# Kernel tuning notes

Measured on AMD Instinct MI355X. Metric: run time of the kernel, lower is better.

The kernel has to match this reference:

```python
import jax, jax.numpy as jnp
import numpy as np

NBINS = 256
NCH = 3


def _channel_hists(img):
    """img: [B, 3, H, W] float with values in [0, 256).
    Returns [3, 256] histogram counts, summed over the batch (matches
    cv2.calcHist per channel accumulated over images)."""
    idx = jnp.clip(img, 0.0, 255.0).astype(jnp.int32)          # bin = floor(v)
    offs = (jnp.arange(NCH, dtype=jnp.int32) * NBINS)[None, :, None, None]
    flat = (idx + offs).reshape(-1)                             # [B*3*H*W]
    h = jnp.zeros(NCH * NBINS, dtype=img.dtype).at[flat].add(1.0)
    return h.reshape(NCH, NBINS)


def _bhattacharyya_sum(h1, h2):
    """OpenCV HISTCMP_BHATTACHARYYA per channel, summed over channels.
    d = sqrt(1 - sum(sqrt(H1*H2)) / (N * sqrt(mean(H1)*mean(H2))))"""
    s = jnp.sum(jnp.sqrt(h1 * h2), axis=-1)                     # [3]
    denom = jnp.sqrt(h1.mean(-1) * h2.mean(-1)) * NBINS         # [3]
    d = jnp.sqrt(jnp.maximum(1.0 - s / denom, 0.0))
    return jnp.sum(d)


def setup_inputs() -> dict:
    key = jax.random.key(0)
    k1, k2 = jax.random.split(key)
    shape = (32, 3, 512, 512)
    # pixel values in [0, 256) like real image data
    inp = jax.random.uniform(k1, shape, dtype=jnp.float32) * 256.0
    lab = jax.random.uniform(k2, shape, dtype=jnp.float32) * 256.0
    return {"input": inp, "label": lab}


def reference(input, label):
    h_in = _channel_hists(input)    # [3, 256]
    h_lb = _channel_hists(label)    # [3, 256]
    return _bhattacharyya_sum(h_in, h_lb)
```

## Files before the change

kernel.cpp:

```cpp
#include <hip/hip_runtime.h>

#define NBINS 256
#define NCH 3
#define NHIST (2 * NCH * NBINS)
#define HW4 65536
#define BATCH 32
#define BLOCKS_PER_JOB 256
#define THREADS 256

__device__ __forceinline__ void batch4(unsigned int* lbase, float4 v) {
    const int b0 = (int)fminf(fmaxf(v.x, 0.f), 255.f);
    const int b1 = (int)fminf(fmaxf(v.y, 0.f), 255.f);
    const int b2 = (int)fminf(fmaxf(v.z, 0.f), 255.f);
    const int b3 = (int)fminf(fmaxf(v.w, 0.f), 255.f);
    const int w0 = b0 >> 2, w1 = b1 >> 2, w2 = b2 >> 2, w3 = b3 >> 2;
    unsigned int i0 = 1u << ((b0 & 3) << 3);
    unsigned int i1 = 1u << ((b1 & 3) << 3);
    unsigned int i2 = 1u << ((b2 & 3) << 3);
    unsigned int i3 = 1u << ((b3 & 3) << 3);
    unsigned int* const p0 = lbase + w0 * 64;
    unsigned int* const p1 = lbase + w1 * 64;
    unsigned int* const p2 = lbase + w2 * 64;
    unsigned int* const p3 = lbase + w3 * 64;
    const unsigned int r0 = *p0;
    const unsigned int r1 = *p1;
    const unsigned int r2 = *p2;
    const unsigned int r3 = *p3;
    if (w0 == w1) { i1 += i0; i0 = 0; }
    if (w0 == w2) { i2 += i0; i0 = 0; }
    if (w0 == w3) { i3 += i0; i0 = 0; }
    if (w1 == w2) { i2 += i1; i1 = 0; }
    if (w1 == w3) { i3 += i1; i1 = 0; }
    if (w2 == w3) { i3 += i2; i2 = 0; }
    *p0 = r0 + i0;
    *p1 = r1 + i1;
    *p2 = r2 + i2;
    *p3 = r3 + i3;
}

__global__ __launch_bounds__(THREADS) void hist_kernel(
    const float* __restrict__ a, const float* __restrict__ b,
    unsigned int* __restrict__ gh) {
    __shared__ unsigned int sh[16384];
    const int tid  = threadIdx.x;
    const int wave = tid >> 6;
    const int lane = tid & 63;

    uint4* shv = (uint4*)sh;
    #pragma unroll
    for (int i = 0; i < 16; ++i)
        shv[tid + i * THREADS] = make_uint4(0u, 0u, 0u, 0u);
    __syncthreads();

    const int job        = blockIdx.x >> 8;
    const int blockInJob = blockIdx.x & 255;
    const int arr = job / NCH;
    const int ch  = job % NCH;

    const float4* __restrict__ src = (const float4*)(arr ? b : a);
    unsigned int* const lbase = &sh[wave * 4096 + lane];
    const unsigned pos = ((unsigned)blockInJob << 8) | (unsigned)tid;

    for (int it = 0; it < BATCH / 4; ++it) {
        const int bt = it << 2;
        const float4 v0 = src[(unsigned)(((bt + 0) * NCH + ch) << 16) | pos];
        const float4 v1 = src[(unsigned)(((bt + 1) * NCH + ch) << 16) | pos];
        const float4 v2 = src[(unsigned)(((bt + 2) * NCH + ch) << 16) | pos];
        const float4 v3 = src[(unsigned)(((bt + 3) * NCH + ch) << 16) | pos];
        batch4(lbase, v0);
        batch4(lbase, v1);
        batch4(lbase, v2);
        batch4(lbase, v3);
    }
    __syncthreads();

    unsigned int sum = 0;
    const int grp = tid >> 2;
    const int sh8 = (tid & 3) << 3;
    #pragma unroll
    for (int w = 0; w < 4; ++w) {
        const unsigned int* base = &sh[w * 4096 + grp * 64];
        #pragma unroll
        for (int c = 0; c < 16; ++c) {
            const int cc = (c + tid) & 15;
            const uint4 q = *(const uint4*)(base + cc * 4);
            sum += ((q.x >> sh8) & 0xFFu) + ((q.y >> sh8) & 0xFFu)
                 + ((q.z >> sh8) & 0xFFu) + ((q.w >> sh8) & 0xFFu);
        }
    }
    atomicAdd(&gh[(arr * NCH + ch) * NBINS + tid], sum);
}

__device__ __forceinline__ double block_reduce256(double v, double* sh4) {
    const int t = threadIdx.x;
    const int lane = t & 63, w = t >> 6;
    #pragma unroll
    for (int o = 32; o > 0; o >>= 1) v += __shfl_down(v, o, 64);
    if (lane == 0) sh4[w] = v;
    __syncthreads();
    double r = sh4[0] + sh4[1] + sh4[2] + sh4[3];
    __syncthreads();
    return r;
}

__global__ __launch_bounds__(256) void bhat_kernel(
    const unsigned int* __restrict__ gh, float* __restrict__ out) {
    __shared__ double sh4[4];
    const int t = threadIdx.x;
    double result = 0.0;
    #pragma unroll
    for (int ch = 0; ch < NCH; ++ch) {
        const double h1 = (double)gh[ch * NBINS + t];
        const double h2 = (double)gh[(NCH + ch) * NBINS + t];
        const double s  = block_reduce256(sqrt(h1 * h2), sh4);
        const double s1 = block_reduce256(h1, sh4);
        const double s2 = block_reduce256(h2, sh4);
        const double denom = sqrt((s1 / (double)NBINS) * (s2 / (double)NBINS)) * (double)NBINS;
        const double v = 1.0 - s / denom;
        result += sqrt(v > 0.0 ? v : 0.0);
    }
    if (t == 0) out[0] = (float)result;
}

extern "C" void kernel_launch(void* const* d_in, const int* in_sizes, int n_in,
                              void* d_out, int out_size, void* d_ws, size_t ws_size,
                              hipStream_t stream) {
    const float* input = (const float*)d_in[0];
    const float* label = (const float*)d_in[1];
    float* out = (float*)d_out;
    unsigned int* gh = (unsigned int*)d_ws;

    hipMemsetAsync(gh, 0, NHIST * sizeof(unsigned int), stream);

    hist_kernel<<<6 * BLOCKS_PER_JOB, THREADS, 0, stream>>>(input, label, gh);
    bhat_kernel<<<1, 256, 0, stream>>>(gh, out);
}
```

Before: 218.5 us.

## Share LDS byte-counter histograms between lane pairs with DPP merge and prefetch

```diff
diff --git a/kernel.cpp b/kernel.cpp
--- a/kernel.cpp
+++ b/kernel.cpp
@@ -4,11 +4,15 @@
 #define NCH 3
 #define NHIST (2 * NCH * NBINS)
 #define HW4 65536
-#define BATCH 32
-#define BLOCKS_PER_JOB 256
+#define BLOCKS_PER_JOB 512
 #define THREADS 256
+#define STEP (2 * NCH * HW4)
 
-__device__ __forceinline__ void batch4(unsigned int* lbase, float4 v) {
+__device__ __forceinline__ int dppswap(int v) {
+    return __builtin_amdgcn_mov_dpp(v, 0xB1, 0xF, 0xF, false);
+}
+
+__device__ __forceinline__ void process4(unsigned int* __restrict__ base, float4 v) {
     const int b0 = (int)fminf(fmaxf(v.x, 0.f), 255.f);
     const int b1 = (int)fminf(fmaxf(v.y, 0.f), 255.f);
     const int b2 = (int)fminf(fmaxf(v.z, 0.f), 255.f);
@@ -18,10 +22,10 @@
     unsigned int i1 = 1u << ((b1 & 3) << 3);
     unsigned int i2 = 1u << ((b2 & 3) << 3);
     unsigned int i3 = 1u << ((b3 & 3) << 3);
-    unsigned int* const p0 = lbase + w0 * 64;
-    unsigned int* const p1 = lbase + w1 * 64;
-    unsigned int* const p2 = lbase + w2 * 64;
-    unsigned int* const p3 = lbase + w3 * 64;
+    unsigned int* const p0 = base + w0 * 32;
+    unsigned int* const p1 = base + w1 * 32;
+    unsigned int* const p2 = base + w2 * 32;
+    unsigned int* const p3 = base + w3 * 32;
     const unsigned int r0 = *p0;
     const unsigned int r1 = *p1;
     const unsigned int r2 = *p2;
@@ -32,63 +36,103 @@
     if (w1 == w2) { i2 += i1; i1 = 0; }
     if (w1 == w3) { i3 += i1; i1 = 0; }
     if (w2 == w3) { i3 += i2; i2 = 0; }
+    const int pw0 = dppswap(w0), pw1 = dppswap(w1);
+    const int pw2 = dppswap(w2), pw3 = dppswap(w3);
+    const unsigned pi0 = (unsigned)dppswap((int)i0);
+    const unsigned pi1 = (unsigned)dppswap((int)i1);
+    const unsigned pi2 = (unsigned)dppswap((int)i2);
+    const unsigned pi3 = (unsigned)dppswap((int)i3);
+    i0 += (w0 == pw0 ? pi0 : 0u) + (w0 == pw1 ? pi1 : 0u)
+        + (w0 == pw2 ? pi2 : 0u) + (w0 == pw3 ? pi3 : 0u);
+    i1 += (w1 == pw0 ? pi0 : 0u) + (w1 == pw1 ? pi1 : 0u)
+        + (w1 == pw2 ? pi2 : 0u) + (w1 == pw3 ? pi3 : 0u);
+    i2 += (w2 == pw0 ? pi0 : 0u) + (w2 == pw1 ? pi1 : 0u)
+        + (w2 == pw2 ? pi2 : 0u) + (w2 == pw3 ? pi3 : 0u);
+    i3 += (w3 == pw0 ? pi0 : 0u) + (w3 == pw1 ? pi1 : 0u)
+        + (w3 == pw2 ? pi2 : 0u) + (w3 == pw3 ? pi3 : 0u);
     *p0 = r0 + i0;
     *p1 = r1 + i1;
     *p2 = r2 + i2;
     *p3 = r3 + i3;
 }
 
-__global__ __launch_bounds__(THREADS) void hist_kernel(
+__global__ __launch_bounds__(THREADS, 5) void hist_kernel(
     const float* __restrict__ a, const float* __restrict__ b,
     unsigned int* __restrict__ gh) {
-    __shared__ unsigned int sh[16384];
+    __shared__ unsigned int sh[8192];
     const int tid  = threadIdx.x;
     const int wave = tid >> 6;
     const int lane = tid & 63;
 
     uint4* shv = (uint4*)sh;
     #pragma unroll
-    for (int i = 0; i < 16; ++i)
+    for (int i = 0; i < 8; ++i)
         shv[tid + i * THREADS] = make_uint4(0u, 0u, 0u, 0u);
     __syncthreads();
 
-    const int job        = blockIdx.x >> 8;
-    const int blockInJob = blockIdx.x & 255;
+    const int job = blockIdx.x / BLOCKS_PER_JOB;
+    const int bij = blockIdx.x % BLOCKS_PER_JOB;
     const int arr = job / NCH;
     const int ch  = job % NCH;
 
-    const float4* __restrict__ src = (const float4*)(arr ? b : a);
-    unsigned int* const lbase = &sh[wave * 4096 + lane];
-    const unsigned pos = ((unsigned)blockInJob << 8) | (unsigned)tid;
+    const float4* __restrict__ src4 = (const float4*)(arr ? b : a);
+    unsigned int* const base = &sh[wave * 2048 + (lane >> 1)];
 
-    for (int it = 0; it < BATCH / 4; ++it) {
-        const int bt = it << 2;
-        const float4 v0 = src[(unsigned)(((bt + 0) * NCH + ch) << 16) | pos];
-        const float4 v1 = src[(unsigned)(((bt + 1) * NCH + ch) << 16) | pos];
-        const float4 v2 = src[(unsigned)(((bt + 2) * NCH + ch) << 16) | pos];
-        const float4 v3 = src[(unsigned)(((bt + 3) * NCH + ch) << 16) | pos];
-        batch4(lbase, v0);
-        batch4(lbase, v1);
-        batch4(lbase, v2);
-        batch4(lbase, v3);
+    const unsigned tg  = ((unsigned)bij << 8) | (unsigned)tid;
+    const unsigned hi  = tg >> 16;
+    const unsigned pos = tg & (HW4 - 1);
+    const unsigned base_idx = hi * (NCH * HW4) + (unsigned)ch * HW4 + pos;
+
+    float4 c0 = src4[base_idx + 0u * STEP];
+    float4 c1 = src4[base_idx + 1u * STEP];
+    float4 c2 = src4[base_idx + 2u * STEP];
+    float4 c3 = src4[base_idx + 3u * STEP];
+    #pragma unroll
+    for (int g2 = 0; g2 < 4; ++g2) {
+        float4 n0, n1, n2, n3;
+        if (g2 < 3) {
+            const unsigned k = (unsigned)(4 * g2 + 4);
+            n0 = src4[base_idx + (k + 0u) * STEP];
+            n1 = src4[base_idx + (k + 1u) * STEP];
+            n2 = src4[base_idx + (k + 2u) * STEP];
+            n3 = src4[base_idx + (k + 3u) * STEP];
+        }
+        process4(base, c0);
+        process4(base, c1);
+        process4(base, c2);
+        process4(base, c3);
+        if (g2 < 3) { c0 = n0; c1 = n1; c2 = n2; c3 = n3; }
     }
     __syncthreads();
 
-    unsigned int sum = 0;
-    const int grp = tid >> 2;
-    const int sh8 = (tid & 3) << 3;
-    #pragma unroll
-    for (int w = 0; w < 4; ++w) {
-        const unsigned int* base = &sh[w * 4096 + grp * 64];
+    {
+        const unsigned int* rbase = &sh[wave * 2048 + lane * 32];
+        unsigned lo = 0u, hiS = 0u;
         #pragma unroll
-        for (int c = 0; c < 16; ++c) {
-            const int cc = (c + tid) & 15;
-            const uint4 q = *(const uint4*)(base + cc * 4);
-            sum += ((q.x >> sh8) & 0xFFu) + ((q.y >> sh8) & 0xFFu)
-                 + ((q.z >> sh8) & 0xFFu) + ((q.w >> sh8) & 0xFFu);
+        for (int c = 0; c < 8; ++c) {
+            const int cc = (c + lane) & 7;
+            const uint4 q = *(const uint4*)(rbase + cc * 4);
+            lo  += (q.x & 0x00FF00FFu) + (q.y & 0x00FF00FFu)
+                 + (q.z & 0x00FF00FFu) + (q.w & 0x00FF00FFu);
+            hiS += ((q.x >> 8) & 0x00FF00FFu) + ((q.y >> 8) & 0x00FF00FFu)
+                 + ((q.z >> 8) & 0x00FF00FFu) + ((q.w >> 8) & 0x00FF00FFu);
         }
+        sh[wave * 2048 + lane]      = lo;
+        sh[wave * 2048 + 64 + lane] = hiS;
     }
-    atomicAdd(&gh[(arr * NCH + ch) * NBINS + tid], sum);
+    __syncthreads();
+
+    {
+        const int g = tid >> 2, byte = tid & 3;
+        const int off = (byte & 1) ? 64 : 0;
+        unsigned s = 0u;
+        #pragma unroll
+        for (int q = 0; q < 4; ++q) {
+            const unsigned v = sh[q * 2048 + off + g];
+            s += (byte & 2) ? (v >> 16) : (v & 0xFFFFu);
+        }
+        atomicAdd(&gh[(arr * NCH + ch) * NBINS + tid], s);
+    }
 }
 
 __device__ __forceinline__ double block_reduce256(double v, double* sh4) {
```

Measured after the change: 226.7 us. 1.04x slower.

## Split histogram into per-array kernels with LDS atomics and prefetched loads

Applied to the files above, without the earlier changes.

```diff
diff --git a/kernel.cpp b/kernel.cpp
--- a/kernel.cpp
+++ b/kernel.cpp
@@ -4,9 +4,87 @@
 #define NCH 3
 #define NHIST (2 * NCH * NBINS)
 #define HW4 65536
-#define BATCH 32
-#define BLOCKS_PER_JOB 256
 #define THREADS 256
+#define BLOCKS_PER_JOB 512
+#define STEP (2 * NCH * HW4)
+
+
+__global__ __launch_bounds__(THREADS) void hist_atomic(
+    const float* __restrict__ src, unsigned int* __restrict__ gh) {
+    __shared__ unsigned int sh[8192];
+    const int tid  = threadIdx.x;
+    const int wave = tid >> 6;
+    const int lane = tid & 63;
+    const int pair = lane >> 1;
+
+    uint4* shv = (uint4*)sh;
+    #pragma unroll
+    for (int i = 0; i < 8; ++i)
+        shv[tid + i * THREADS] = make_uint4(0u, 0u, 0u, 0u);
+    __syncthreads();
+
+    const int ch  = blockIdx.x / BLOCKS_PER_JOB;
+    const int bij = blockIdx.x % BLOCKS_PER_JOB;
+
+    const float4* __restrict__ src4 = (const float4*)src;
+    unsigned int* const base = &sh[wave * 2048 + pair * 64];
+
+    const unsigned tg  = ((unsigned)bij << 8) | (unsigned)tid;
+    const unsigned hi  = tg >> 16;
+    const unsigned pos = tg & (HW4 - 1);
+    const unsigned base_idx = hi * (NCH * HW4) + (unsigned)ch * HW4 + pos;
+
+    #define ATOM1(x) do { \
+        const int _b = (int)fminf(fmaxf((x), 0.f), 255.f); \
+        atomicAdd(&base[_b >> 2], 1u << ((_b & 3) << 3)); } while (0)
+    #define ATOM4(v) do { ATOM1((v).x); ATOM1((v).y); ATOM1((v).z); ATOM1((v).w); } while (0)
+
+    float4 c0 = src4[base_idx + 0u * STEP];
+    float4 c1 = src4[base_idx + 1u * STEP];
+    float4 c2 = src4[base_idx + 2u * STEP];
+    float4 c3 = src4[base_idx + 3u * STEP];
+    #pragma unroll
+    for (int g2 = 0; g2 < 4; ++g2) {
+        float4 n0, n1, n2, n3;
+        if (g2 < 3) {
+            const unsigned k = (unsigned)(4 * g2 + 4);
+            n0 = src4[base_idx + (k + 0u) * STEP];
+            n1 = src4[base_idx + (k + 1u) * STEP];
+            n2 = src4[base_idx + (k + 2u) * STEP];
+            n3 = src4[base_idx + (k + 3u) * STEP];
+        }
+        ATOM4(c0); ATOM4(c1); ATOM4(c2); ATOM4(c3);
+        if (g2 < 3) { c0 = n0; c1 = n1; c2 = n2; c3 = n3; }
+    }
+    __syncthreads();
+
+    {
+        const unsigned int* rb = &sh[wave * 2048];
+        unsigned lo = 0u, hiS = 0u;
+        #pragma unroll
+        for (int p = 0; p < 32; ++p) {
+            const int pp = (p + lane) & 31;
+            const unsigned v = rb[pp * 64 + lane];
+            lo  += v & 0x00FF00FFu;
+            hiS += (v >> 8) & 0x00FF00FFu;
+        }
+        sh[wave * 2048 + lane]      = lo;
+        sh[wave * 2048 + 64 + lane] = hiS;
+    }
+    __syncthreads();
+
+    {
+        const int grp = tid >> 2, byte = tid & 3;
+        const int off = (byte & 1) ? 64 : 0;
+        unsigned s = 0u;
+        #pragma unroll
+        for (int q = 0; q < 4; ++q) {
+            const unsigned v = sh[q * 2048 + off + grp];
+            s += (byte & 2) ? (v >> 16) : (v & 0xFFFFu);
+        }
+        atomicAdd(&gh[ch * NBINS + tid], s);
+    }
+}
 
 __device__ __forceinline__ void batch4(unsigned int* lbase, float4 v) {
     const int b0 = (int)fminf(fmaxf(v.x, 0.f), 255.f);
@@ -38,9 +116,8 @@
     *p3 = r3 + i3;
 }
 
-__global__ __launch_bounds__(THREADS) void hist_kernel(
-    const float* __restrict__ a, const float* __restrict__ b,
-    unsigned int* __restrict__ gh) {
+__global__ __launch_bounds__(THREADS) void hist_rmw(
+    const float* __restrict__ src, unsigned int* __restrict__ gh) {
     __shared__ unsigned int sh[16384];
     const int tid  = threadIdx.x;
     const int wave = tid >> 6;
@@ -52,25 +129,36 @@
         shv[tid + i * THREADS] = make_uint4(0u, 0u, 0u, 0u);
     __syncthreads();
 
-    const int job        = blockIdx.x >> 8;
-    const int blockInJob = blockIdx.x & 255;
-    const int arr = job / NCH;
-    const int ch  = job % NCH;
-
-    const float4* __restrict__ src = (const float4*)(arr ? b : a);
+    const int ch  = blockIdx.x / BLOCKS_PER_JOB;
+    const int bij = blockIdx.x % BLOCKS_PER_JOB;
+
+    const float4* __restrict__ src4 = (const float4*)src;
     unsigned int* const lbase = &sh[wave * 4096 + lane];
-    const unsigned pos = ((unsigned)blockInJob << 8) | (unsigned)tid;
-
-    for (int it = 0; it < BATCH / 4; ++it) {
-        const int bt = it << 2;
-        const float4 v0 = src[(unsigned)(((bt + 0) * NCH + ch) << 16) | pos];
-        const float4 v1 = src[(unsigned)(((bt + 1) * NCH + ch) << 16) | pos];
-        const float4 v2 = src[(unsigned)(((bt + 2) * NCH + ch) << 16) | pos];
-        const float4 v3 = src[(unsigned)(((bt + 3) * NCH + ch) << 16) | pos];
-        batch4(lbase, v0);
-        batch4(lbase, v1);
-        batch4(lbase, v2);
-        batch4(lbase, v3);
+
+    const unsigned tg  = ((unsigned)bij << 8) | (unsigned)tid;
+    const unsigned hi  = tg >> 16;
+    const unsigned pos = tg & (HW4 - 1);
+    const unsigned base_idx = hi * (NCH * HW4) + (unsigned)ch * HW4 + pos;
+
+    float4 c0 = src4[base_idx + 0u * STEP];
+    float4 c1 = src4[base_idx + 1u * STEP];
+    float4 c2 = src4[base_idx + 2u * STEP];
+    float4 c3 = src4[base_idx + 3u * STEP];
+    #pragma unroll
+    for (int g2 = 0; g2 < 4; ++g2) {
+        float4 n0, n1, n2, n3;
+        if (g2 < 3) {
+            const unsigned k = (unsigned)(4 * g2 + 4);
+            n0 = src4[base_idx + (k + 0u) * STEP];
+            n1 = src4[base_idx + (k + 1u) * STEP];
+            n2 = src4[base_idx + (k + 2u) * STEP];
+            n3 = src4[base_idx + (k + 3u) * STEP];
+        }
+        batch4(lbase, c0);
+        batch4(lbase, c1);
+        batch4(lbase, c2);
+        batch4(lbase, c3);
+        if (g2 < 3) { c0 = n0; c1 = n1; c2 = n2; c3 = n3; }
     }
     __syncthreads();
 
@@ -88,7 +176,7 @@
                  + ((q.z >> sh8) & 0xFFu) + ((q.w >> sh8) & 0xFFu);
         }
     }
-    atomicAdd(&gh[(arr * NCH + ch) * NBINS + tid], sum);
+    atomicAdd(&gh[(NCH + ch) * NBINS + tid], sum);
 }
 
 __device__ __forceinline__ double block_reduce256(double v, double* sh4) {
@@ -132,6 +220,7 @@
 
     hipMemsetAsync(gh, 0, NHIST * sizeof(unsigned int), stream);
 
-    hist_kernel<<<6 * BLOCKS_PER_JOB, THREADS, 0, stream>>>(input, label, gh);
+    hist_atomic<<<NCH * BLOCKS_PER_JOB, THREADS, 0, stream>>>(input, gh);
+    hist_rmw   <<<NCH * BLOCKS_PER_JOB, THREADS, 0, stream>>>(label, gh);
     bhat_kernel<<<1, 256, 0, stream>>>(gh, out);
 }
```

Result: slower. 229.5 us (+5.0%).

## Split histogram work between LDS packed counters and per-wave global atomic copies

Applied to the files above, without the earlier changes.

```diff
diff --git a/kernel.cpp b/kernel.cpp
--- a/kernel.cpp
+++ b/kernel.cpp
@@ -4,9 +4,14 @@
 #define NCH 3
 #define NHIST (2 * NCH * NBINS)
 #define HW4 65536
-#define BATCH 32
-#define BLOCKS_PER_JOB 256
 #define THREADS 256
+#define BLOCKS_PER_JOB 512
+#define NJOBS 6
+#define STEP (2 * NCH * HW4)
+#define WAVES_PER_JOB (BLOCKS_PER_JOB * 4)
+#define NCOPIES (NJOBS * WAVES_PER_JOB)
+#define PRIV_OFF 2048
+
 
 __device__ __forceinline__ void batch4(unsigned int* lbase, float4 v) {
     const int b0 = (int)fminf(fmaxf(v.x, 0.f), 255.f);
@@ -38,9 +43,16 @@
     *p3 = r3 + i3;
 }
 
+__device__ __forceinline__ void gatom4(unsigned int* __restrict__ g, float4 v) {
+    atomicAdd(&g[(int)fminf(fmaxf(v.x, 0.f), 255.f)], 1u);
+    atomicAdd(&g[(int)fminf(fmaxf(v.y, 0.f), 255.f)], 1u);
+    atomicAdd(&g[(int)fminf(fmaxf(v.z, 0.f), 255.f)], 1u);
+    atomicAdd(&g[(int)fminf(fmaxf(v.w, 0.f), 255.f)], 1u);
+}
+
 __global__ __launch_bounds__(THREADS) void hist_kernel(
     const float* __restrict__ a, const float* __restrict__ b,
-    unsigned int* __restrict__ gh) {
+    unsigned int* __restrict__ priv, unsigned int* __restrict__ gh) {
     __shared__ unsigned int sh[16384];
     const int tid  = threadIdx.x;
     const int wave = tid >> 6;
@@ -52,25 +64,40 @@
         shv[tid + i * THREADS] = make_uint4(0u, 0u, 0u, 0u);
     __syncthreads();
 
-    const int job        = blockIdx.x >> 8;
-    const int blockInJob = blockIdx.x & 255;
+    const int job = blockIdx.x >> 9;
+    const int bij = blockIdx.x & 511;
     const int arr = job / NCH;
     const int ch  = job % NCH;
 
-    const float4* __restrict__ src = (const float4*)(arr ? b : a);
+    const float4* __restrict__ src4 = (const float4*)(arr ? b : a);
     unsigned int* const lbase = &sh[wave * 4096 + lane];
-    const unsigned pos = ((unsigned)blockInJob << 8) | (unsigned)tid;
+    unsigned int* const gpriv =
+        priv + ((unsigned)(job * WAVES_PER_JOB + (bij << 2) + wave)) * NBINS;
 
-    for (int it = 0; it < BATCH / 4; ++it) {
-        const int bt = it << 2;
-        const float4 v0 = src[(unsigned)(((bt + 0) * NCH + ch) << 16) | pos];
-        const float4 v1 = src[(unsigned)(((bt + 1) * NCH + ch) << 16) | pos];
-        const float4 v2 = src[(unsigned)(((bt + 2) * NCH + ch) << 16) | pos];
-        const float4 v3 = src[(unsigned)(((bt + 3) * NCH + ch) << 16) | pos];
-        batch4(lbase, v0);
-        batch4(lbase, v1);
-        batch4(lbase, v2);
-        batch4(lbase, v3);
+    const unsigned tg  = ((unsigned)bij << 8) | (unsigned)tid;
+    const unsigned hi  = tg >> 16;
+    const unsigned pos = tg & (HW4 - 1);
+    const unsigned base_idx = hi * (NCH * HW4) + (unsigned)ch * HW4 + pos;
+
+    float4 c0 = src4[base_idx + 0u * STEP];
+    float4 c1 = src4[base_idx + 1u * STEP];
+    float4 c2 = src4[base_idx + 2u * STEP];
+    float4 c3 = src4[base_idx + 3u * STEP];
+    #pragma unroll
+    for (int g2 = 0; g2 < 4; ++g2) {
+        float4 n0, n1, n2, n3;
+        if (g2 < 3) {
+            const unsigned k = (unsigned)(4 * g2 + 4);
+            n0 = src4[base_idx + (k + 0u) * STEP];
+            n1 = src4[base_idx + (k + 1u) * STEP];
+            n2 = src4[base_idx + (k + 2u) * STEP];
+            n3 = src4[base_idx + (k + 3u) * STEP];
+        }
+        batch4(lbase, c0);
+        batch4(lbase, c1);
+        batch4(lbase, c2);
+        gatom4(gpriv, c3);
+        if (g2 < 3) { c0 = n0; c1 = n1; c2 = n2; c3 = n3; }
     }
     __syncthreads();
 
@@ -88,7 +115,29 @@
                  + ((q.z >> sh8) & 0xFFu) + ((q.w >> sh8) & 0xFFu);
         }
     }
-    atomicAdd(&gh[(arr * NCH + ch) * NBINS + tid], sum);
+    atomicAdd(&gh[job * NBINS + tid], sum);
+}
+
+__global__ __launch_bounds__(256) void merge_kernel(
+    const unsigned int* __restrict__ priv, unsigned int* __restrict__ gh) {
+    const int job   = blockIdx.x >> 4;
+    const int slice = blockIdx.x & 15;
+    const unsigned int* base =
+        priv + (unsigned)(job * WAVES_PER_JOB + slice * 128) * NBINS + threadIdx.x;
+    unsigned s0 = 0, s1 = 0, s2 = 0, s3 = 0, s4 = 0, s5 = 0, s6 = 0, s7 = 0;
+    #pragma unroll 4
+    for (int c = 0; c < 128; c += 8) {
+        s0 += base[(c + 0) * NBINS];
+        s1 += base[(c + 1) * NBINS];
+        s2 += base[(c + 2) * NBINS];
+        s3 += base[(c + 3) * NBINS];
+        s4 += base[(c + 4) * NBINS];
+        s5 += base[(c + 5) * NBINS];
+        s6 += base[(c + 6) * NBINS];
+        s7 += base[(c + 7) * NBINS];
+    }
+    const unsigned s = ((s0 + s1) + (s2 + s3)) + ((s4 + s5) + (s6 + s7));
+    atomicAdd(&gh[job * NBINS + threadIdx.x], s);
 }
 
 __device__ __forceinline__ double block_reduce256(double v, double* sh4) {
@@ -128,10 +177,14 @@
     const float* input = (const float*)d_in[0];
     const float* label = (const float*)d_in[1];
     float* out = (float*)d_out;
-    unsigned int* gh = (unsigned int*)d_ws;
+    unsigned int* gh   = (unsigned int*)d_ws;
+    unsigned int* priv = (unsigned int*)d_ws + PRIV_OFF;
 
-    hipMemsetAsync(gh, 0, NHIST * sizeof(unsigned int), stream);
+    hipMemsetAsync(d_ws, 0,
+                   (size_t)(PRIV_OFF + NCOPIES * NBINS) * sizeof(unsigned int),
+                   stream);
 
-    hist_kernel<<<6 * BLOCKS_PER_JOB, THREADS, 0, stream>>>(input, label, gh);
-    bhat_kernel<<<1, 256, 0, stream>>>(gh, out);
+    hist_kernel <<<NJOBS * BLOCKS_PER_JOB, THREADS, 0, stream>>>(input, label, priv, gh);
+    merge_kernel<<<NJOBS * 16, 256, 0, stream>>>(priv, gh);
+    bhat_kernel <<<1, 256, 0, stream>>>(gh, out);
 }
```

Measured after the change: 409.2 us. +87.2%, slower.
